# Optimization experiments

Measured on AMD Instinct MI355X. Metric: run time of the kernel, lower is better.

Reference implementation:

```python
import jax, jax.numpy as jnp
import numpy as np

B, S, D, H = 8, 512, 1024, 16
DK = D // H          # 64
N_ASP = 4            # aspect tokens per sample
NEG = -1000000000.0


def setup_inputs() -> dict:
    key = jax.random.key(0)
    ks = jax.random.split(key, 12)
    return {
        "query": jax.random.normal(ks[0], (B, S, D), jnp.float32),
        "key_in": jax.random.normal(ks[1], (B, S, D), jnp.float32),
        "mask": jax.random.randint(ks[2], (B, S, S), 0, 2).astype(jnp.int32),
        "aspect": jax.random.normal(ks[3], (B, 1, D), jnp.float32),
        "aspect_ids": jax.random.randint(ks[4], (B, N_ASP), 0, S),
        # learned params
        "Wq": jax.random.normal(ks[5], (D, D), jnp.float32) / np.sqrt(D).astype(np.float32),
        "bq": jnp.zeros((D,), jnp.float32),
        "Wk": jax.random.normal(ks[6], (D, D), jnp.float32) / np.sqrt(D).astype(np.float32),
        "bk": jnp.zeros((D,), jnp.float32),
        "Wd": jax.random.normal(ks[7], (D, DK), jnp.float32) / np.sqrt(D).astype(np.float32),
        "bd": jnp.zeros((DK,), jnp.float32),
        "weight_m": jax.random.normal(ks[8], (H, DK, DK), jnp.float32) / np.sqrt(DK).astype(np.float32),
        "bias_m": jnp.zeros((1,), jnp.float32),
    }


def reference(query, key_in, mask, aspect, aspect_ids,
              Wq, bq, Wk, bk, Wd, bd, weight_m, bias_m):
    # projections -> [B,H,S,DK]
    q = (query @ Wq + bq).reshape(B, S, H, DK).transpose(0, 2, 1, 3)
    k = (key_in @ Wk + bk).reshape(B, S, H, DK).transpose(0, 2, 1, 3)

    # aspect -> dense -> broadcast to [B,H,S,DK]
    asp = aspect @ Wd + bd                                  # [B,1,DK]
    asp = jnp.broadcast_to(asp[:, None, :, :], (B, H, S, DK))

    # asps = tanh(aspect @ W_m @ K^T + bias_m)  -> [B,H,S,S]
    aw = jnp.einsum('bhsd,hde->bhse', asp, weight_m)
    asps = jnp.tanh(jnp.einsum('bhse,bhte->bhst', aw, k) + bias_m[0])

    # per-(batch,head) average score vector over rows -> [B,H,S]
    avg = asps.sum(axis=-2) / S

    # scatter: for each aspect index, overwrite its row and column with avg
    # (sequential over the small fixed N_ASP, matching torch write order:
    #  row write then column write per index)
    a_sc = asps
    bidx = jnp.arange(B)
    for j in range(N_ASP):
        idx = aspect_ids[:, j]                              # [B]
        a_sc = a_sc.at[bidx, :, idx, :].set(avg)            # rows
        a_sc = a_sc.at[bidx, :, :, idx].set(avg)            # cols

    # standard masked attention probs
    scores = jnp.einsum('bhsd,bhtd->bhst', q, k) / np.float32(np.sqrt(DK))
    scores = jnp.where(mask[:, None, :, :] == 0, NEG, scores)
    attn = jax.nn.softmax(scores, axis=-1)
    return a_sc, attn
```

## Files before the change

### kernel.cpp

```cpp
#include <hip/hip_runtime.h>

typedef __bf16 bf16x8 __attribute__((ext_vector_type(8)));
typedef float  f32x4  __attribute__((ext_vector_type(4)));

__device__ __forceinline__ unsigned short f2bf(float f) {
  union { float f; unsigned u; } x; x.f = f;
  unsigned r = (x.u + 0x7FFFu + ((x.u >> 16) & 1u)) >> 16;
  return (unsigned short)r;
}

__device__ __forceinline__ void gload_lds16(const void* g, void* l) {
  __builtin_amdgcn_global_load_lds((__attribute__((address_space(1))) void*)g,
                                   (__attribute__((address_space(3))) void*)l,
                                   16, 0, 0);
}

__global__ void conv_kernel(const float* __restrict__ a, const float* __restrict__ b,
                            unsigned short* __restrict__ ao, unsigned short* __restrict__ bo,
                            int n4) {
  int i = blockIdx.x * 256 + threadIdx.x;
  if (i < n4) {
    float4 x = ((const float4*)a)[i];
    ushort4 y; y.x = f2bf(x.x); y.y = f2bf(x.y); y.z = f2bf(x.z); y.w = f2bf(x.w);
    ((ushort4*)ao)[i] = y;
  } else {
    int j = i - n4;
    float4 x = ((const float4*)b)[j];
    ushort4 y; y.x = f2bf(x.x); y.y = f2bf(x.y); y.z = f2bf(x.z); y.w = f2bf(x.w);
    ((ushort4*)bo)[j] = y;
  }
}

__global__ void wtrans_kernel(const float* __restrict__ Wq, const float* __restrict__ Wk,
                              unsigned short* __restrict__ Wqt, unsigned short* __restrict__ Wkt) {
  const float* W = blockIdx.z ? Wk : Wq;
  unsigned short* Wt = blockIdx.z ? Wkt : Wqt;
  __shared__ unsigned short tile[32][33];
  int k0 = blockIdx.x * 32, n0 = blockIdx.y * 32;
  int tx = threadIdx.x, ty = threadIdx.y;
  #pragma unroll
  for (int i = 0; i < 4; ++i) {
    int k = ty + i * 8;
    tile[k][tx] = f2bf(W[(size_t)(k0 + k) * 1024 + n0 + tx]);
  }
  __syncthreads();
  #pragma unroll
  for (int i = 0; i < 4; ++i) {
    int n = ty + i * 8;
    Wt[(size_t)(n0 + n) * 1024 + k0 + tx] = tile[tx][n];
  }
}

__global__ __launch_bounds__(256)
void prep_aw_kernel(const float* __restrict__ aspect, const float* __restrict__ Wd,
                    const float* __restrict__ bd, const float* __restrict__ weight_m,
                    const float* __restrict__ bk,
                    float* __restrict__ aw_out, float* __restrict__ c_out) {
  int bh = blockIdx.x, b = bh >> 4, h = bh & 15;
  int tid = threadIdx.x, e = tid & 63, g = tid >> 6;
  __shared__ float part[4][64];
  __shared__ float asp_s[64];
  __shared__ float aw_s[64];
  const float* arow = aspect + (size_t)b * 1024;
  float acc = 0.f;
  for (int d = g * 256; d < g * 256 + 256; ++d)
    acc += arow[d] * Wd[(size_t)d * 64 + e];
  part[g][e] = acc;
  __syncthreads();
  if (tid < 64)
    asp_s[tid] = bd[tid] + part[0][tid] + part[1][tid] + part[2][tid] + part[3][tid];
  __syncthreads();
  if (tid < 64) {
    const float* wm = weight_m + (size_t)h * 4096;
    float aw = 0.f;
    #pragma unroll 8
    for (int d = 0; d < 64; ++d) aw += asp_s[d] * wm[d * 64 + tid];
    aw_s[tid] = aw;
    aw_out[(size_t)bh * 64 + tid] = aw;
  }
  __syncthreads();
  if (g == 0) {
    float s = bk[h * 64 + e] * aw_s[e];
    #pragma unroll
    for (int off = 32; off >= 1; off >>= 1) s += __shfl_xor(s, off, 64);
    if (e == 0) c_out[bh] = s;
  }
}

__global__ __launch_bounds__(256)
void prep_u_kernel(const float* __restrict__ Wk, const float* __restrict__ aw_in,
                   float* __restrict__ u_out) {
  int bh = blockIdx.y, h = bh & 15;
  int dbase = blockIdx.x * 128;
  int tid = threadIdx.x, e = tid & 63, g = tid >> 6;
  float awl = aw_in[(size_t)bh * 64 + e];
  #pragma unroll 4
  for (int it = 0; it < 16; ++it) {
    int d0 = dbase + g * 32 + it * 2;
    float s0 = Wk[(size_t)d0 * 1024 + h * 64 + e] * awl;
    float s1 = Wk[(size_t)(d0 + 1) * 1024 + h * 64 + e] * awl;
    #pragma unroll
    for (int off = 32; off >= 1; off >>= 1) {
      s0 += __shfl_xor(s0, off, 64);
      s1 += __shfl_xor(s1, off, 64);
    }
    if (e == 0) {
      u_out[(size_t)bh * 1024 + d0]     = s0;
      u_out[(size_t)bh * 1024 + d0 + 1] = s1;
    }
  }
}

__global__ void bitmask_kernel(const int* __restrict__ mask, unsigned long long* __restrict__ mb) {
  int gw = (blockIdx.x * 256 + threadIdx.x) >> 6;
  int lane = threadIdx.x & 63;
  for (int row = gw; row < 4096; row += 1024) {
    const int* mr = mask + (size_t)row * 512;
    unsigned long long* dst = mb + (size_t)row * 8;
    #pragma unroll
    for (int it = 0; it < 8; ++it) {
      int m = mr[it * 64 + lane];
      unsigned long long bb = __ballot(m != 0);
      if (lane == 0) dst[it] = bb;
    }
  }
}

__global__ __launch_bounds__(256)
void v_kernel(const float* __restrict__ key_in, const float* __restrict__ u,
              const float* __restrict__ c, const float* __restrict__ bias_m,
              float* __restrict__ v) {
  __shared__ float ks_[8][1024];
  int b = blockIdx.y, t0 = blockIdx.x * 8;
  int tid = threadIdx.x, wid = tid >> 6, lane = tid & 63;
  const float4* ksrc = (const float4*)(key_in + ((size_t)b * 512 + t0) * 1024);
  float4* kdst = (float4*)&ks_[0][0];
  for (int i = tid; i < 2048; i += 256) kdst[i] = ksrc[i];
  __syncthreads();
  const float* ub = u + (size_t)b * 16384;
  int r0 = wid * 2;
  float acc0[16] = {}, acc1[16] = {};
  for (int i = 0; i < 16; ++i) {
    int col = lane + 64 * i;
    float kv0 = ks_[r0][col], kv1 = ks_[r0 + 1][col];
    #pragma unroll
    for (int h = 0; h < 16; ++h) {
      float uv = ub[h * 1024 + col];
      acc0[h] += kv0 * uv;
      acc1[h] += kv1 * uv;
    }
  }
  float cb = bias_m[0];
  #pragma unroll
  for (int h = 0; h < 16; ++h) {
    float a0 = acc0[h], a1 = acc1[h];
    #pragma unroll
    for (int off = 32; off >= 1; off >>= 1) {
      a0 += __shfl_xor(a0, off, 64);
      a1 += __shfl_xor(a1, off, 64);
    }
    if (lane == h) {
      int bh = b * 16 + h;
      float cc = c[bh] + cb;
      v[(size_t)bh * 512 + t0 + r0]     = tanhf(a0 + cc);
      v[(size_t)bh * 512 + t0 + r0 + 1] = tanhf(a1 + cc);
    }
  }
}

__global__ void asc_kernel(const float* __restrict__ v, const int* __restrict__ ids,
                           float* __restrict__ out) {
  size_t i4 = (size_t)blockIdx.x * 256 + threadIdx.x;
  int t0 = (int)(i4 & 127) * 4;
  int s  = (int)(i4 >> 7) & 511;
  int bh = (int)(i4 >> 16);
  int b  = bh >> 4;
  int i0 = ids[b * 4], i1 = ids[b * 4 + 1], i2 = ids[b * 4 + 2], i3 = ids[b * 4 + 3];
  #define LASTOF(t) ((i3==(t))?3:(i2==(t))?2:(i1==(t))?1:(i0==(t))?0:-1)
  int ls  = LASTOF(s);
  int lt0 = LASTOF(t0), lt1 = LASTOF(t0+1), lt2 = LASTOF(t0+2), lt3 = LASTOF(t0+3);
  #undef LASTOF
  const float* vrow = v + (size_t)bh * 512;
  float vs = vrow[s];
  float4 vt = *(const float4*)(vrow + t0);
  f32x4 o;
  o[0] = (lt0 >= 0 && lt0 >= ls) ? vs : vt.x;
  o[1] = (lt1 >= 0 && lt1 >= ls) ? vs : vt.y;
  o[2] = (lt2 >= 0 && lt2 >= ls) ? vs : vt.z;
  o[3] = (lt3 >= 0 && lt3 >= ls) ? vs : vt.w;
  __builtin_nontemporal_store(o, ((f32x4*)out) + i4);
}

__global__ __launch_bounds__(256, 2)
void gemm_kernel(const unsigned short* __restrict__ Aq, const unsigned short* __restrict__ Ak,
                 const unsigned short* __restrict__ Bq, const unsigned short* __restrict__ Bk,
                 const float* __restrict__ bq, const float* __restrict__ bk,
                 unsigned short* __restrict__ qb, unsigned short* __restrict__ kb) {
  const unsigned short* A  = blockIdx.z ? Ak : Aq;
  const unsigned short* Bt = blockIdx.z ? Bk : Bq;
  const float* bias = blockIdx.z ? bk : bq;
  unsigned short* out = blockIdx.z ? kb : qb;
  const int m0 = blockIdx.x * 128, n0 = blockIdx.y * 128;
  __shared__ __align__(16) unsigned short As[128 * 64];
  __shared__ __align__(16) unsigned short Bs[128 * 64];
  const int tid = threadIdx.x, wid = tid >> 6, lane = tid & 63;
  const int wr = wid >> 1, wc = wid & 1;
  const int quad = lane >> 4, l15 = lane & 15;
  const int srw = lane >> 3;
  const int jcol = ((lane & 7) ^ srw) * 8;
  const int p0 = (quad ^ (l15 & 7)) * 8;
  f32x4 acc[4][4] = {};
  for (int k0 = 0; k0 < 1024; k0 += 64) {
    #pragma unroll
    for (int i = 0; i < 4; ++i) {
      int r = wid * 32 + i * 8 + srw;
      gload_lds16(A  + (size_t)(m0 + r) * 1024 + k0 + jcol, As + (wid * 32 + i * 8) * 64);
      gload_lds16(Bt + (size_t)(n0 + r) * 1024 + k0 + jcol, Bs + (wid * 32 + i * 8) * 64);
    }
    __syncthreads();
    bf16x8 af[4][2], bfr[4][2];
    #pragma unroll
    for (int mi = 0; mi < 4; ++mi) {
      const unsigned short* base = As + (wr * 64 + mi * 16 + l15) * 64;
      af[mi][0] = *(const bf16x8*)(base + p0);
      af[mi][1] = *(const bf16x8*)(base + (p0 ^ 32));
    }
    #pragma unroll
    for (int ni = 0; ni < 4; ++ni) {
      const unsigned short* base = Bs + (wc * 64 + ni * 16 + l15) * 64;
      bfr[ni][0] = *(const bf16x8*)(base + p0);
      bfr[ni][1] = *(const bf16x8*)(base + (p0 ^ 32));
    }
    #pragma unroll
    for (int mi = 0; mi < 4; ++mi)
      #pragma unroll
      for (int ni = 0; ni < 4; ++ni) {
        acc[mi][ni] = __builtin_amdgcn_mfma_f32_16x16x32_bf16(af[mi][0], bfr[ni][0], acc[mi][ni], 0, 0, 0);
        acc[mi][ni] = __builtin_amdgcn_mfma_f32_16x16x32_bf16(af[mi][1], bfr[ni][1], acc[mi][ni], 0, 0, 0);
      }
    __syncthreads();
  }
  #pragma unroll
  for (int mi = 0; mi < 4; ++mi) {
    #pragma unroll
    for (int ni = 0; ni < 4; ++ni) {
      const int n = n0 + wc * 64 + ni * 16 + l15;
      const int hh = n >> 6, dk = n & 63;
      const float bv = bias[n];
      #pragma unroll
      for (int r = 0; r < 4; ++r) {
        const int m = m0 + wr * 64 + mi * 16 + quad * 4 + r;
        const int bb = m >> 9, ss = m & 511;
        out[(((size_t)bb * 16 + hh) * 512 + ss) * 64 + dk] = f2bf(acc[mi][ni][r] + bv);
      }
    }
  }
}

__global__ __launch_bounds__(256, 2)
void attn_kernel(const unsigned short* __restrict__ qb, const unsigned short* __restrict__ kb,
                 const unsigned* __restrict__ mbits, float* __restrict__ attn) {
  __shared__ __align__(16) unsigned short ks[256 * 64];
  __shared__ __align__(16) unsigned short qs[64 * 64];
  const int bh = blockIdx.x, b = bh >> 4;
  const int s0 = blockIdx.y * 64;
  const int tid = threadIdx.x, wid = tid >> 6, lane = tid & 63;
  const int quad = lane >> 4, l15 = lane & 15;
  const int srw = lane >> 3;
  const int j8 = ((lane & 7) ^ srw) * 8;
  const int p0 = (quad ^ (l15 & 7)) * 8;
  const unsigned short* kslab = kb + (size_t)bh * 512 * 64;
  const unsigned short* qslab = qb + ((size_t)bh * 512 + s0) * 64;
  #pragma unroll
  for (int i = 0; i < 2; ++i)
    gload_lds16(qslab + (wid * 2 + i) * 512 + srw * 64 + j8, qs + (wid * 2 + i) * 512);
  #pragma unroll
  for (int i = 0; i < 8; ++i)
    gload_lds16(kslab + (wid * 8 + i) * 512 + srw * 64 + j8, ks + (wid * 8 + i) * 512);
  __syncthreads();
  const unsigned short* qbase = qs + (wid * 16 + l15) * 64;
  bf16x8 af0 = *(const bf16x8*)(qbase + p0);
  bf16x8 af1 = *(const bf16x8*)(qbase + (p0 ^ 32));
  f32x4 acc[32];
  #pragma unroll
  for (int tile = 0; tile < 16; ++tile) {
    const unsigned short* kbase = ks + (tile * 16 + l15) * 64;
    bf16x8 b0 = *(const bf16x8*)(kbase + p0);
    bf16x8 b1 = *(const bf16x8*)(kbase + (p0 ^ 32));
    f32x4 a = {0.f, 0.f, 0.f, 0.f};
    a = __builtin_amdgcn_mfma_f32_16x16x32_bf16(af0, b0, a, 0, 0, 0);
    a = __builtin_amdgcn_mfma_f32_16x16x32_bf16(af1, b1, a, 0, 0, 0);
    acc[tile] = a;
  }
  __syncthreads();
  #pragma unroll
  for (int i = 0; i < 8; ++i)
    gload_lds16(kslab + 16384 + (wid * 8 + i) * 512 + srw * 64 + j8, ks + (wid * 8 + i) * 512);
  __syncthreads();
  #pragma unroll
  for (int tile = 16; tile < 32; ++tile) {
    const unsigned short* kbase = ks + ((tile - 16) * 16 + l15) * 64;
    bf16x8 b0 = *(const bf16x8*)(kbase + p0);
    bf16x8 b1 = *(const bf16x8*)(kbase + (p0 ^ 32));
    f32x4 a = {0.f, 0.f, 0.f, 0.f};
    a = __builtin_amdgcn_mfma_f32_16x16x32_bf16(af0, b0, a, 0, 0, 0);
    a = __builtin_amdgcn_mfma_f32_16x16x32_bf16(af1, b1, a, 0, 0, 0);
    acc[tile] = a;
  }
  const size_t srow = (size_t)s0 + wid * 16 + quad * 4;
  const unsigned* mrow = mbits + ((size_t)b * 512 + srow) * 16;
  float mx[4] = {-3.0e38f, -3.0e38f, -3.0e38f, -3.0e38f};
  #pragma unroll
  for (int tp = 0; tp < 16; ++tp) {
    #pragma unroll
    for (int r = 0; r < 4; ++r) {
      unsigned m = mrow[(size_t)r * 16 + tp];
      float sc0 = acc[2 * tp][r] * 0.125f;
      float sc1 = acc[2 * tp + 1][r] * 0.125f;
      sc0 = ((m >> l15) & 1u) ? sc0 : -1.0e9f;
      sc1 = ((m >> (16 + l15)) & 1u) ? sc1 : -1.0e9f;
      acc[2 * tp][r] = sc0;
      acc[2 * tp + 1][r] = sc1;
      mx[r] = fmaxf(mx[r], fmaxf(sc0, sc1));
    }
  }
  #pragma unroll
  for (int r = 0; r < 4; ++r)
    #pragma unroll
    for (int off = 1; off < 16; off <<= 1)
      mx[r] = fmaxf(mx[r], __shfl_xor(mx[r], off, 64));
  float sm[4] = {0.f, 0.f, 0.f, 0.f};
  #pragma unroll
  for (int tile = 0; tile < 32; ++tile)
    #pragma unroll
    for (int r = 0; r < 4; ++r) {
      float e = __expf(acc[tile][r] - mx[r]);
      acc[tile][r] = e;
      sm[r] += e;
    }
  #pragma unroll
  for (int r = 0; r < 4; ++r) {
    #pragma unroll
    for (int off = 1; off < 16; off <<= 1)
      sm[r] += __shfl_xor(sm[r], off, 64);
    sm[r] = 1.0f / sm[r];
  }
  float* obase = attn + ((size_t)bh * 512 + srow) * 512 + l15;
  #pragma unroll
  for (int r = 0; r < 4; ++r)
    #pragma unroll
    for (int tile = 0; tile < 32; ++tile)
      __builtin_nontemporal_store(acc[tile][r] * sm[r], &obase[(size_t)r * 512 + tile * 16]);
}

extern "C" void kernel_launch(void* const* d_in, const int* in_sizes, int n_in,
                              void* d_out, int out_size, void* d_ws, size_t ws_size,
                              hipStream_t stream) {
  const float* query    = (const float*)d_in[0];
  const float* key_in   = (const float*)d_in[1];
  const int*   mask     = (const int*)d_in[2];
  const float* aspect   = (const float*)d_in[3];
  const int*   a_ids    = (const int*)d_in[4];
  const float* Wq       = (const float*)d_in[5];
  const float* bq       = (const float*)d_in[6];
  const float* Wk       = (const float*)d_in[7];
  const float* bk       = (const float*)d_in[8];
  const float* Wd       = (const float*)d_in[9];
  const float* bd       = (const float*)d_in[10];
  const float* weight_m = (const float*)d_in[11];
  const float* bias_m   = (const float*)d_in[12];

  float* out_asc  = (float*)d_out;
  float* out_attn = out_asc + 33554432ull;

  char* ws = (char*)d_ws;
  unsigned short* Aq   = (unsigned short*)(ws);
  unsigned short* Ak   = (unsigned short*)(ws + 8388608);
  unsigned short* Wqt  = (unsigned short*)(ws + 16777216);
  unsigned short* Wkt  = (unsigned short*)(ws + 18874368);
  unsigned short* qbuf = (unsigned short*)(ws + 20971520);
  unsigned short* kbuf = (unsigned short*)(ws + 29360128);
  float* u   = (float*)(ws + 37748736);
  float* c   = (float*)(ws + 38273024);
  float* v   = (float*)(ws + 38277120);
  unsigned long long* mb = (unsigned long long*)(ws + 38539264);
  float* aw  = (float*)(ws + 38801408);

  conv_kernel<<<dim3(8192), dim3(256), 0, stream>>>(query, key_in, Aq, Ak, 1048576);
  wtrans_kernel<<<dim3(32, 32, 2), dim3(32, 8), 0, stream>>>(Wq, Wk, Wqt, Wkt);
  prep_aw_kernel<<<dim3(128), dim3(256), 0, stream>>>(aspect, Wd, bd, weight_m, bk, aw, c);
  bitmask_kernel<<<dim3(256), dim3(256), 0, stream>>>(mask, mb);
  prep_u_kernel<<<dim3(8, 128), dim3(256), 0, stream>>>(Wk, aw, u);
  gemm_kernel<<<dim3(32, 8, 2), dim3(256), 0, stream>>>(Aq, Ak, Wqt, Wkt, bq, bk, qbuf, kbuf);
  v_kernel<<<dim3(64, 8), dim3(256), 0, stream>>>(key_in, u, c, bias_m, v);
  asc_kernel<<<dim3(32768), dim3(256), 0, stream>>>(v, a_ids, out_asc);
  attn_kernel<<<dim3(128, 8), dim3(256), 0, stream>>>(qbuf, kbuf, (const unsigned*)mb, out_attn);
}
```

Before: 425.2 us.

## Fuse prep kernels into one launch and load full K slab in attention

Merges the bf16 conversion, weight transpose, mask bitpacking, aspect projection and u-vector kernels into a single block-indexed launch. The aw projection is now recomputed per block instead of round-tripping through global memory. The attention kernel now loads the whole 512-row K slab into LDS at once, which removes the mid-kernel barrier and reload. In exchange its LDS footprint doubles to about 72KB, which may limit occupancy under the two-blocks launch bound.

```diff
diff --git a/kernel.cpp b/kernel.cpp
--- a/kernel.cpp
+++ b/kernel.cpp
@@ -15,113 +15,113 @@
                                    16, 0, 0);
 }
 
-__global__ void conv_kernel(const float* __restrict__ a, const float* __restrict__ b,
-                            unsigned short* __restrict__ ao, unsigned short* __restrict__ bo,
-                            int n4) {
-  int i = blockIdx.x * 256 + threadIdx.x;
-  if (i < n4) {
-    float4 x = ((const float4*)a)[i];
-    ushort4 y; y.x = f2bf(x.x); y.y = f2bf(x.y); y.z = f2bf(x.z); y.w = f2bf(x.w);
-    ((ushort4*)ao)[i] = y;
+__global__ __launch_bounds__(256)
+void prep_fused_kernel(const float* __restrict__ query, const float* __restrict__ key_in,
+                       const float* __restrict__ Wq, const float* __restrict__ Wk,
+                       const float* __restrict__ aspect, const float* __restrict__ Wd,
+                       const float* __restrict__ bd, const float* __restrict__ weight_m,
+                       const float* __restrict__ bk, const int* __restrict__ mask,
+                       unsigned short* __restrict__ Aq, unsigned short* __restrict__ Ak,
+                       unsigned short* __restrict__ Wqt, unsigned short* __restrict__ Wkt,
+                       float* __restrict__ u_out, float* __restrict__ c_out,
+                       unsigned long long* __restrict__ mb) {
+  __shared__ __align__(16) char smem[2112];
+  const int bx = blockIdx.x, tid = threadIdx.x;
+  if (bx < 8192) {
+    int i = bx * 256 + tid;
+    if (i < 1048576) {
+      float4 x = ((const float4*)query)[i];
+      ushort4 y; y.x = f2bf(x.x); y.y = f2bf(x.y); y.z = f2bf(x.z); y.w = f2bf(x.w);
+      ((ushort4*)Aq)[i] = y;
+    } else {
+      int j = i - 1048576;
+      float4 x = ((const float4*)key_in)[j];
+      ushort4 y; y.x = f2bf(x.x); y.y = f2bf(x.y); y.z = f2bf(x.z); y.w = f2bf(x.w);
+      ((ushort4*)Ak)[j] = y;
+    }
+  } else if (bx < 10240) {
+    int t = bx - 8192;
+    const float* W = (t >> 10) ? Wk : Wq;
+    unsigned short* Wt = (t >> 10) ? Wkt : Wqt;
+    int tile_id = t & 1023;
+    int k0 = (tile_id & 31) * 32, n0 = (tile_id >> 5) * 32;
+    int tx = tid & 31, ty = tid >> 5;
+    unsigned short (*tile)[33] = (unsigned short (*)[33])smem;
+    #pragma unroll
+    for (int i = 0; i < 4; ++i) {
+      int k = ty + i * 8;
+      tile[k][tx] = f2bf(W[(size_t)(k0 + k) * 1024 + n0 + tx]);
+    }
+    __syncthreads();
+    #pragma unroll
+    for (int i = 0; i < 4; ++i) {
+      int n = ty + i * 8;
+      Wt[(size_t)(n0 + n) * 1024 + k0 + tx] = tile[tx][n];
+    }
+  } else if (bx < 10496) {
+    int t = bx - 10240;
+    int gw = (t * 256 + tid) >> 6, lane = tid & 63;
+    for (int row = gw; row < 4096; row += 1024) {
+      const int* mr = mask + (size_t)row * 512;
+      unsigned long long* dst = mb + (size_t)row * 8;
+      #pragma unroll
+      for (int it = 0; it < 8; ++it) {
+        int m = mr[it * 64 + lane];
+        unsigned long long bb = __ballot(m != 0);
+        if (lane == 0) dst[it] = bb;
+      }
+    }
   } else {
-    int j = i - n4;
-    float4 x = ((const float4*)b)[j];
-    ushort4 y; y.x = f2bf(x.x); y.y = f2bf(x.y); y.z = f2bf(x.z); y.w = f2bf(x.w);
-    ((ushort4*)bo)[j] = y;
-  }
-}
-
-__global__ void wtrans_kernel(const float* __restrict__ Wq, const float* __restrict__ Wk,
-                              unsigned short* __restrict__ Wqt, unsigned short* __restrict__ Wkt) {
-  const float* W = blockIdx.z ? Wk : Wq;
-  unsigned short* Wt = blockIdx.z ? Wkt : Wqt;
-  __shared__ unsigned short tile[32][33];
-  int k0 = blockIdx.x * 32, n0 = blockIdx.y * 32;
-  int tx = threadIdx.x, ty = threadIdx.y;
-  #pragma unroll
-  for (int i = 0; i < 4; ++i) {
-    int k = ty + i * 8;
-    tile[k][tx] = f2bf(W[(size_t)(k0 + k) * 1024 + n0 + tx]);
-  }
-  __syncthreads();
-  #pragma unroll
-  for (int i = 0; i < 4; ++i) {
-    int n = ty + i * 8;
-    Wt[(size_t)(n0 + n) * 1024 + k0 + tx] = tile[tx][n];
-  }
-}
-
-__global__ __launch_bounds__(256)
-void prep_aw_kernel(const float* __restrict__ aspect, const float* __restrict__ Wd,
-                    const float* __restrict__ bd, const float* __restrict__ weight_m,
-                    const float* __restrict__ bk,
-                    float* __restrict__ aw_out, float* __restrict__ c_out) {
-  int bh = blockIdx.x, b = bh >> 4, h = bh & 15;
-  int tid = threadIdx.x, e = tid & 63, g = tid >> 6;
-  __shared__ float part[4][64];
-  __shared__ float asp_s[64];
-  __shared__ float aw_s[64];
-  const float* arow = aspect + (size_t)b * 1024;
-  float acc = 0.f;
-  for (int d = g * 256; d < g * 256 + 256; ++d)
-    acc += arow[d] * Wd[(size_t)d * 64 + e];
-  part[g][e] = acc;
-  __syncthreads();
-  if (tid < 64)
-    asp_s[tid] = bd[tid] + part[0][tid] + part[1][tid] + part[2][tid] + part[3][tid];
-  __syncthreads();
-  if (tid < 64) {
-    const float* wm = weight_m + (size_t)h * 4096;
-    float aw = 0.f;
-    #pragma unroll 8
-    for (int d = 0; d < 64; ++d) aw += asp_s[d] * wm[d * 64 + tid];
-    aw_s[tid] = aw;
-    aw_out[(size_t)bh * 64 + tid] = aw;
-  }
-  __syncthreads();
-  if (g == 0) {
-    float s = bk[h * 64 + e] * aw_s[e];
-    #pragma unroll
-    for (int off = 32; off >= 1; off >>= 1) s += __shfl_xor(s, off, 64);
-    if (e == 0) c_out[bh] = s;
-  }
-}
-
-__global__ __launch_bounds__(256)
-void prep_u_kernel(const float* __restrict__ Wk, const float* __restrict__ aw_in,
-                   float* __restrict__ u_out) {
-  int bh = blockIdx.y, h = bh & 15;
-  int dbase = blockIdx.x * 128;
-  int tid = threadIdx.x, e = tid & 63, g = tid >> 6;
-  float awl = aw_in[(size_t)bh * 64 + e];
-  #pragma unroll 4
-  for (int it = 0; it < 16; ++it) {
-    int d0 = dbase + g * 32 + it * 2;
-    float s0 = Wk[(size_t)d0 * 1024 + h * 64 + e] * awl;
-    float s1 = Wk[(size_t)(d0 + 1) * 1024 + h * 64 + e] * awl;
-    #pragma unroll
-    for (int off = 32; off >= 1; off >>= 1) {
-      s0 += __shfl_xor(s0, off, 64);
-      s1 += __shfl_xor(s1, off, 64);
-    }
-    if (e == 0) {
-      u_out[(size_t)bh * 1024 + d0]     = s0;
-      u_out[(size_t)bh * 1024 + d0 + 1] = s1;
-    }
-  }
-}
-
-__global__ void bitmask_kernel(const int* __restrict__ mask, unsigned long long* __restrict__ mb) {
-  int gw = (blockIdx.x * 256 + threadIdx.x) >> 6;
-  int lane = threadIdx.x & 63;
-  for (int row = gw; row < 4096; row += 1024) {
-    const int* mr = mask + (size_t)row * 512;
-    unsigned long long* dst = mb + (size_t)row * 8;
-    #pragma unroll
-    for (int it = 0; it < 8; ++it) {
-      int m = mr[it * 64 + lane];
-      unsigned long long bb = __ballot(m != 0);
-      if (lane == 0) dst[it] = bb;
+    int id = bx - 10496;
+    int bh = id >> 1, b = bh >> 4, h = bh & 15;
+    int dbase = (id & 1) * 512;
+    int e = tid & 63, g = tid >> 6;
+    float* part  = (float*)smem;
+    float* asp_s = part + 256;
+    float* aw_s  = asp_s + 64;
+    const float* arow = aspect + (size_t)b * 1024;
+    float acc = 0.f;
+    for (int d = g * 256; d < g * 256 + 256; ++d)
+      acc += arow[d] * Wd[(size_t)d * 64 + e];
+    part[g * 64 + e] = acc;
+    __syncthreads();
+    if (tid < 64)
+      asp_s[tid] = bd[tid] + part[tid] + part[64 + tid] + part[128 + tid] + part[192 + tid];
+    __syncthreads();
+    if (tid < 64) {
+      const float* wm = weight_m + (size_t)h * 4096;
+      float aw = 0.f;
+      #pragma unroll 8
+      for (int d = 0; d < 64; ++d) aw += asp_s[d] * wm[d * 64 + tid];
+      aw_s[tid] = aw;
+    }
+    __syncthreads();
+    float awl = aw_s[e];
+    if ((id & 1) == 0 && g == 0) {
+      float s = bk[h * 64 + e] * awl;
+      #pragma unroll
+      for (int off = 32; off >= 1; off >>= 1) s += __shfl_xor(s, off, 64);
+      if (e == 0) c_out[bh] = s;
+    }
+    const float* wkcol = Wk + h * 64 + e;
+    #pragma unroll 2
+    for (int it = 0; it < 32; ++it) {
+      int d0 = dbase + g * 128 + it * 4;
+      float s0 = wkcol[(size_t)d0 * 1024] * awl;
+      float s1 = wkcol[(size_t)(d0 + 1) * 1024] * awl;
+      float s2 = wkcol[(size_t)(d0 + 2) * 1024] * awl;
+      float s3 = wkcol[(size_t)(d0 + 3) * 1024] * awl;
+      #pragma unroll
+      for (int off = 32; off >= 1; off >>= 1) {
+        s0 += __shfl_xor(s0, off, 64);
+        s1 += __shfl_xor(s1, off, 64);
+        s2 += __shfl_xor(s2, off, 64);
+        s3 += __shfl_xor(s3, off, 64);
+      }
+      if (e == 0) {
+        float4 uo = {s0, s1, s2, s3};
+        *(float4*)(u_out + (size_t)bh * 1024 + d0) = uo;
+      }
     }
   }
 }
@@ -260,7 +260,7 @@
 __global__ __launch_bounds__(256, 2)
 void attn_kernel(const unsigned short* __restrict__ qb, const unsigned short* __restrict__ kb,
                  const unsigned* __restrict__ mbits, float* __restrict__ attn) {
-  __shared__ __align__(16) unsigned short ks[256 * 64];
+  __shared__ __align__(16) unsigned short ks[512 * 64];
   __shared__ __align__(16) unsigned short qs[64 * 64];
   const int bh = blockIdx.x, b = bh >> 4;
   const int s0 = blockIdx.y * 64;
@@ -275,31 +275,16 @@
   for (int i = 0; i < 2; ++i)
     gload_lds16(qslab + (wid * 2 + i) * 512 + srw * 64 + j8, qs + (wid * 2 + i) * 512);
   #pragma unroll
-  for (int i = 0; i < 8; ++i)
-    gload_lds16(kslab + (wid * 8 + i) * 512 + srw * 64 + j8, ks + (wid * 8 + i) * 512);
+  for (int i = 0; i < 16; ++i)
+    gload_lds16(kslab + (wid * 16 + i) * 512 + srw * 64 + j8, ks + (wid * 16 + i) * 512);
   __syncthreads();
   const unsigned short* qbase = qs + (wid * 16 + l15) * 64;
   bf16x8 af0 = *(const bf16x8*)(qbase + p0);
   bf16x8 af1 = *(const bf16x8*)(qbase + (p0 ^ 32));
   f32x4 acc[32];
   #pragma unroll
-  for (int tile = 0; tile < 16; ++tile) {
+  for (int tile = 0; tile < 32; ++tile) {
     const unsigned short* kbase = ks + (tile * 16 + l15) * 64;
-    bf16x8 b0 = *(const bf16x8*)(kbase + p0);
-    bf16x8 b1 = *(const bf16x8*)(kbase + (p0 ^ 32));
-    f32x4 a = {0.f, 0.f, 0.f, 0.f};
-    a = __builtin_amdgcn_mfma_f32_16x16x32_bf16(af0, b0, a, 0, 0, 0);
-    a = __builtin_amdgcn_mfma_f32_16x16x32_bf16(af1, b1, a, 0, 0, 0);
-    acc[tile] = a;
-  }
-  __syncthreads();
-  #pragma unroll
-  for (int i = 0; i < 8; ++i)
-    gload_lds16(kslab + 16384 + (wid * 8 + i) * 512 + srw * 64 + j8, ks + (wid * 8 + i) * 512);
-  __syncthreads();
-  #pragma unroll
-  for (int tile = 16; tile < 32; ++tile) {
-    const unsigned short* kbase = ks + ((tile - 16) * 16 + l15) * 64;
     bf16x8 b0 = *(const bf16x8*)(kbase + p0);
     bf16x8 b1 = *(const bf16x8*)(kbase + (p0 ^ 32));
     f32x4 a = {0.f, 0.f, 0.f, 0.f};
@@ -384,13 +369,10 @@
   float* c   = (float*)(ws + 38273024);
   float* v   = (float*)(ws + 38277120);
   unsigned long long* mb = (unsigned long long*)(ws + 38539264);
-  float* aw  = (float*)(ws + 38801408);
-
-  conv_kernel<<<dim3(8192), dim3(256), 0, stream>>>(query, key_in, Aq, Ak, 1048576);
-  wtrans_kernel<<<dim3(32, 32, 2), dim3(32, 8), 0, stream>>>(Wq, Wk, Wqt, Wkt);
-  prep_aw_kernel<<<dim3(128), dim3(256), 0, stream>>>(aspect, Wd, bd, weight_m, bk, aw, c);
-  bitmask_kernel<<<dim3(256), dim3(256), 0, stream>>>(mask, mb);
-  prep_u_kernel<<<dim3(8, 128), dim3(256), 0, stream>>>(Wk, aw, u);
+
+  prep_fused_kernel<<<dim3(10752), dim3(256), 0, stream>>>(
+      query, key_in, Wq, Wk, aspect, Wd, bd, weight_m, bk, mask,
+      Aq, Ak, Wqt, Wkt, u, c, mb);
   gemm_kernel<<<dim3(32, 8, 2), dim3(256), 0, stream>>>(Aq, Ak, Wqt, Wkt, bq, bk, qbuf, kbuf);
   v_kernel<<<dim3(64, 8), dim3(256), 0, stream>>>(key_in, u, c, bias_m, v);
   asc_kernel<<<dim3(32768), dim3(256), 0, stream>>>(v, a_ids, out_asc);
```

Result: slower. 464.3 us (+9.2%).
